# Performance work log

Hardware: AMD Instinct MI355X
Metric: run time of the kernel (lower is better)

## Reference

```python
import jax, jax.numpy as jnp
import numpy as np

EMBED_DIM = 256
NUM_HEADS = 8
HEAD_DIM = EMBED_DIM // NUM_HEADS
NUM_GRAPHS = 64
MAX_LEN = 512
EPS = 1e-5
SCALE = float(1.0 / np.sqrt(HEAD_DIM))


def setup_inputs() -> dict:
    rng = np.random.default_rng(0)
    lengths = rng.integers(256, MAX_LEN + 1, size=NUM_GRAPHS)  # variable graph sizes
    batch = jnp.asarray(np.repeat(np.arange(NUM_GRAPHS), lengths), dtype=jnp.int32)
    N = int(lengths.sum())
    key = jax.random.key(0)
    ks = jax.random.split(key, 4)
    s = float(1.0 / np.sqrt(EMBED_DIM))
    return dict(
        x=jax.random.normal(ks[0], (N, EMBED_DIM), jnp.float32),
        batch=batch,
        in_proj_w=jax.random.uniform(ks[1], (3 * EMBED_DIM, EMBED_DIM), jnp.float32, -s, s),
        in_proj_b=jnp.zeros((3 * EMBED_DIM,), jnp.float32),
        out_proj_w=jax.random.uniform(ks[2], (EMBED_DIM, EMBED_DIM), jnp.float32, -s, s),
        out_proj_b=jnp.zeros((EMBED_DIM,), jnp.float32),
        ln_weight=jnp.ones((EMBED_DIM,), jnp.float32),
        ln_bias=jnp.zeros((EMBED_DIM,), jnp.float32),
    )


def reference(x, batch, in_proj_w, in_proj_b, out_proj_w, out_proj_b, ln_weight, ln_bias):
    N, D = x.shape
    # --- to_dense_batch: pad variable-size graphs into [B, S, D] ---
    counts = jax.ops.segment_sum(jnp.ones((N,), jnp.int32), batch, num_segments=NUM_GRAPHS)
    starts = jnp.cumsum(counts) - counts
    pos = jnp.arange(N, dtype=jnp.int32) - starts[batch]  # position of node inside its graph
    dense = jnp.zeros((NUM_GRAPHS, MAX_LEN, D), x.dtype).at[batch, pos].set(x)
    mask = jnp.zeros((NUM_GRAPHS, MAX_LEN), bool).at[batch, pos].set(True)

    # --- masked multi-head self-attention (torch nn.MultiheadAttention semantics) ---
    qkv = dense @ in_proj_w.T + in_proj_b                      # [B, S, 3D]
    q, k, v = jnp.split(qkv, 3, axis=-1)
    hd = lambda t: t.reshape(NUM_GRAPHS, MAX_LEN, NUM_HEADS, HEAD_DIM)
    q, k, v = hd(q), hd(k), hd(v)
    scores = jnp.einsum('bqhd,bkhd->bhqk', q, k) * SCALE       # [B, H, S, S]
    scores = jnp.where(mask[:, None, None, :], scores, -1e9)   # key_padding_mask
    attn = jax.nn.softmax(scores, axis=-1)
    ctx = jnp.einsum('bhqk,bkhd->bqhd', attn, v).reshape(NUM_GRAPHS, MAX_LEN, D)
    out_dense = ctx @ out_proj_w.T + out_proj_b

    # --- gather back to ragged layout + residual ---
    h = out_dense[batch, pos] + x                              # [N, D]

    # --- PyG LayerNorm(mode='graph'): normalize over all nodes & channels per graph ---
    norm = jnp.clip(counts.astype(x.dtype), 1.0)[:, None] * D
    mean = jax.ops.segment_sum(h, batch, num_segments=NUM_GRAPHS).sum(-1, keepdims=True) / norm
    hc = h - mean[batch]
    var = jax.ops.segment_sum(hc * hc, batch, num_segments=NUM_GRAPHS).sum(-1, keepdims=True) / norm
    out = hc / jnp.sqrt(var + EPS)[batch]
    out = out * ln_weight + ln_bias

    # --- activation: exact (erf) GELU, matching torch nn.GELU default ---
    return jax.nn.gelu(out, approximate=False)
```

## Files before the change

### kernel.cpp

```cpp
#include <hip/hip_runtime.h>
#include <hip/hip_bf16.h>
#include <math.h>

#define D_EMB 256
#define NHEAD 8
#define HD 32
#define NG 64
#define QSC 0.25503486f

typedef __attribute__((ext_vector_type(8))) short short8b;
typedef __attribute__((ext_vector_type(4))) float f32x4;

__device__ __forceinline__ unsigned int pk2(float a, float b) {
    union { __hip_bfloat162 t; unsigned int u; } r;
    r.t = __float22bfloat162_rn(make_float2(a, b));
    return r.u;
}

__device__ __forceinline__ short8b pack2v(f32x4 a, f32x4 b) {
    union { unsigned int u[4]; short8b s; } r;
    r.u[0] = pk2(a[0], a[1]);
    r.u[1] = pk2(a[2], a[3]);
    r.u[2] = pk2(b[0], b[1]);
    r.u[3] = pk2(b[2], b[3]);
    return r.s;
}

__device__ __forceinline__ float fexp2(float x) {
    float r;
    asm("v_exp_f32 %0, %1" : "=v"(r) : "v"(x));
    return r;
}

__device__ __forceinline__ void barrier_lgkm() {
    asm volatile("s_waitcnt lgkmcnt(0)" ::: "memory");
    __builtin_amdgcn_s_barrier();
}

__global__ void k_init(const float* __restrict__ x, unsigned short* __restrict__ xb, int n4x,
                       const float* __restrict__ w1, unsigned short* __restrict__ wb1,
                       const float* __restrict__ w2, unsigned short* __restrict__ wb2,
                       const int* __restrict__ batch, int n, int* __restrict__ starts,
                       float* __restrict__ part) {
    int seg = blockIdx.y;
    int i = blockIdx.x * 256 + threadIdx.x;
    if (seg == 3) {
        if (i < n) {
            int b = batch[i];
            if (i == 0 || batch[i - 1] != b) starts[b] = i;
            if (i == n - 1) starts[NG] = n;
        }
        if (blockIdx.x == 0 && threadIdx.x < 128) part[threadIdx.x] = 0.f;
        return;
    }
    const float* src = seg == 0 ? x : (seg == 1 ? w1 : w2);
    unsigned short* dst = seg == 0 ? xb : (seg == 1 ? wb1 : wb2);
    int n4 = seg == 0 ? n4x : (seg == 1 ? 768 * 64 : 256 * 64);
    if (i >= n4) return;
    float4 v = ((const float4*)src)[i];
    uint2 o;
    o.x = pk2(v.x, v.y);
    o.y = pk2(v.z, v.w);
    ((uint2*)dst)[i] = o;
}

#define GLSW 72

template<int MODE>
__global__ __launch_bounds__(256) void k_gemm(
    const unsigned short* __restrict__ A, const unsigned short* __restrict__ W,
    const float* __restrict__ bias, const float* __restrict__ resid,
    float* __restrict__ Cf, unsigned short* __restrict__ Qb,
    unsigned short* __restrict__ Kb, unsigned short* __restrict__ Vb,
    const int* __restrict__ batch, float* __restrict__ part,
    int M, int Ncols) {
    __shared__ __align__(16) unsigned short Al[128][GLSW];
    __shared__ __align__(16) unsigned short Bl[128][GLSW];

    int tid = threadIdx.x;
    int wave = tid >> 6, lane = tid & 63;
    int lrow = lane & 15, lgrp = lane >> 4;
    int wr = wave >> 1, wc = wave & 1;
    int row0 = blockIdx.x * 128, col0 = blockIdx.y * 128;

    int sr = tid >> 3, sc = (tid & 7) * 8;
    int arow[4], brow[4];
#pragma unroll
    for (int p = 0; p < 4; ++p) {
        int r = sr + p * 32;
        int ar = row0 + r; if (ar >= M) ar = M - 1;
        arow[p] = ar;
        brow[p] = col0 + r;
    }

    f32x4 acc[4][4];
#pragma unroll
    for (int i = 0; i < 4; ++i)
#pragma unroll
        for (int j = 0; j < 4; ++j) acc[i][j] = (f32x4){0.f, 0.f, 0.f, 0.f};

    short8b pa[4], pb[4];
#pragma unroll
    for (int p = 0; p < 4; ++p) {
        pa[p] = *(const short8b*)&A[(size_t)arow[p] * 256 + sc];
        pb[p] = *(const short8b*)&W[(size_t)brow[p] * 256 + sc];
    }

    for (int k0 = 0; k0 < 256; k0 += 64) {
#pragma unroll
        for (int p = 0; p < 4; ++p) {
            int r = sr + p * 32;
            *(short8b*)&Al[r][sc] = pa[p];
            *(short8b*)&Bl[r][sc] = pb[p];
        }
        if (k0 + 64 < 256) {
#pragma unroll
            for (int p = 0; p < 4; ++p) {
                pa[p] = *(const short8b*)&A[(size_t)arow[p] * 256 + k0 + 64 + sc];
                pb[p] = *(const short8b*)&W[(size_t)brow[p] * 256 + k0 + 64 + sc];
            }
        }
        barrier_lgkm();
#pragma unroll
        for (int half = 0; half < 2; ++half) {
            short8b af[4], bf[4];
#pragma unroll
            for (int mi = 0; mi < 4; ++mi)
                af[mi] = *(const short8b*)&Al[wr * 64 + mi * 16 + lrow][half * 32 + lgrp * 8];
#pragma unroll
            for (int ni = 0; ni < 4; ++ni)
                bf[ni] = *(const short8b*)&Bl[wc * 64 + ni * 16 + lrow][half * 32 + lgrp * 8];
#pragma unroll
            for (int mi = 0; mi < 4; ++mi)
#pragma unroll
                for (int ni = 0; ni < 4; ++ni)
                    acc[mi][ni] = __builtin_amdgcn_mfma_f32_16x16x32_bf16(
                        af[mi], bf[ni], acc[mi][ni], 0, 0, 0);
        }
        barrier_lgkm();
    }

    if (MODE == 0) {
        int g0 = batch[row0 < M ? row0 : M - 1];
        int rlast = row0 + 127; if (rlast >= M) rlast = M - 1;
        int g1 = batch[rlast];
        float bv[4];
#pragma unroll
        for (int ni = 0; ni < 4; ++ni)
            bv[ni] = bias[col0 + wc * 64 + ni * 16 + lrow];
        float sA = 0.f, qA = 0.f, sB = 0.f, qB = 0.f;
#pragma unroll
        for (int mi = 0; mi < 4; ++mi) {
            int rowb = row0 + wr * 64 + mi * 16 + lgrp * 4;
#pragma unroll
            for (int r = 0; r < 4; ++r) {
                int row = rowb + r;
                if (row >= M) continue;
                float rs = 0.f, rq = 0.f;
#pragma unroll
                for (int ni = 0; ni < 4; ++ni) {
                    int col = col0 + wc * 64 + ni * 16 + lrow;
                    float v = acc[mi][ni][r] + bv[ni];
                    v += resid[(size_t)row * Ncols + col];
                    Cf[(size_t)row * Ncols + col] = v;
                    rs += v;
                    rq += v * v;
                }
                if (batch[row] == g0) { sA += rs; qA += rq; }
                else                  { sB += rs; qB += rq; }
            }
        }
#pragma unroll
        for (int o = 32; o > 0; o >>= 1) {
            sA += __shfl_down(sA, o); qA += __shfl_down(qA, o);
            sB += __shfl_down(sB, o); qB += __shfl_down(qB, o);
        }
        __shared__ float red[4][4];
        if (lane == 0) {
            red[wave][0] = sA; red[wave][1] = qA;
            red[wave][2] = sB; red[wave][3] = qB;
        }
        __syncthreads();
        if (tid == 0) {
            float tA = 0.f, uA = 0.f, tB = 0.f, uB = 0.f;
#pragma unroll
            for (int w = 0; w < 4; ++w) {
                tA += red[w][0]; uA += red[w][1];
                tB += red[w][2]; uB += red[w][3];
            }
            atomicAdd(&part[2 * g0], tA);
            atomicAdd(&part[2 * g0 + 1], uA);
            if (g1 != g0) {
                atomicAdd(&part[2 * g1], tB);
                atomicAdd(&part[2 * g1 + 1], uB);
            }
        }
    } else {
        int sel = blockIdx.y >> 1;
        unsigned short* dst = sel == 0 ? Qb : (sel == 1 ? Kb : Vb);
        float qsc = sel == 0 ? QSC : 1.f;
#pragma unroll
        for (int ni = 0; ni < 4; ++ni) {
            int colg = col0 + wc * 64 + ni * 16 + lrow;
            int col = colg & 255;
            float bvv = bias[colg];
#pragma unroll
            for (int mi = 0; mi < 4; ++mi) {
                int rowb = row0 + wr * 64 + mi * 16 + lgrp * 4;
#pragma unroll
                for (int r = 0; r < 4; ++r) {
                    int row = rowb + r;
                    if (row < M) {
                        union { __hip_bfloat16 b; unsigned short u; } cv;
                        cv.b = __float2bfloat16((acc[mi][ni][r] + bvv) * qsc);
                        dst[(size_t)row * 256 + col] = cv.u;
                    }
                }
            }
        }
    }
}

#define KSW 40
#define VSW 76

__global__ __launch_bounds__(256) void k_attn6(
    const unsigned short* __restrict__ Qb, const unsigned short* __restrict__ Kb,
    const unsigned short* __restrict__ Vb, const int* __restrict__ starts,
    unsigned short* __restrict__ ctxb) {
    int g = blockIdx.x, h = blockIdx.y, chunk = blockIdx.z;
    int s0 = starts[g];
    int L = starts[g + 1] - s0;
    if (chunk * 128 >= L) return;

    __shared__ __align__(16) unsigned short Klds[2][64][KSW];
    __shared__ __align__(16) unsigned short Vt[2][32][VSW];

    int tid = threadIdx.x;
    int wave = tid >> 6, lane = tid & 63;
    int lrow = lane & 15, lgrp = lane >> 4;
    int qbase = chunk * 128 + wave * 32;

    short8b qf[2];
#pragma unroll
    for (int qm = 0; qm < 2; ++qm) {
        int qr = qbase + qm * 16 + lrow;
        if (qr >= L) qr = L - 1;
        qf[qm] = *(const short8b*)&Qb[(size_t)(s0 + qr) * 256 + h * 32 + lgrp * 8];
    }

    int skey = tid >> 2, skc = (tid & 3) * 8;
    int vu = tid >> 3, vd4 = (tid & 7) * 4;

    short8b kreg;
    ushort4 vreg0, vreg1;
    {
        int kr = skey < L ? skey : L - 1;
        kreg = *(const short8b*)&Kb[(size_t)(s0 + kr) * 256 + h * 32 + skc];
        int v0 = (2 * vu) < L ? (2 * vu) : L - 1;
        int v1 = (2 * vu + 1) < L ? (2 * vu + 1) : L - 1;
        vreg0 = *(const ushort4*)&Vb[(size_t)(s0 + v0) * 256 + h * 32 + vd4];
        vreg1 = *(const ushort4*)&Vb[(size_t)(s0 + v1) * 256 + h * 32 + vd4];
    }

    float lrun[2] = {0.f, 0.f};
    f32x4 acc[2][2];
#pragma unroll
    for (int a = 0; a < 2; ++a) {
        acc[a][0] = (f32x4){0.f, 0.f, 0.f, 0.f};
        acc[a][1] = (f32x4){0.f, 0.f, 0.f, 0.f};
    }

    int nkt = (L + 63) >> 6;
    for (int t = 0; t < nkt; ++t) {
        int kt = t * 64;
        int buf = t & 1;

        *(short8b*)&Klds[buf][skey][skc] = kreg;
#pragma unroll
        for (int j = 0; j < 4; ++j) {
            unsigned int pr = (unsigned int)(unsigned short)(&vreg0.x)[j] |
                              ((unsigned int)(unsigned short)(&vreg1.x)[j] << 16);
            *(unsigned int*)&Vt[buf][vd4 + j][2 * vu] = pr;
        }

        if (t + 1 < nkt) {
            int ktn = kt + 64;
            int kr = (ktn + skey) < L ? (ktn + skey) : L - 1;
            kreg = *(const short8b*)&Kb[(size_t)(s0 + kr) * 256 + h * 32 + skc];
            int v0 = (ktn + 2 * vu) < L ? (ktn + 2 * vu) : L - 1;
            int v1 = (ktn + 2 * vu + 1) < L ? (ktn + 2 * vu + 1) : L - 1;
            vreg0 = *(const ushort4*)&Vb[(size_t)(s0 + v0) * 256 + h * 32 + vd4];
            vreg1 = *(const ushort4*)&Vb[(size_t)(s0 + v1) * 256 + h * 32 + vd4];
        }

        barrier_lgkm();

        short8b kf[4];
#pragma unroll
        for (int kn = 0; kn < 4; ++kn)
            kf[kn] = *(const short8b*)&Klds[buf][kn * 16 + lrow][lgrp * 8];
        short8b vf[2][2];
#pragma unroll
        for (int dsub = 0; dsub < 2; ++dsub)
#pragma unroll
            for (int kh = 0; kh < 2; ++kh) {
                ushort4 lo = *(const ushort4*)&Vt[buf][dsub * 16 + lrow][kh * 32 + lgrp * 4];
                ushort4 hi = *(const ushort4*)&Vt[buf][dsub * 16 + lrow][kh * 32 + 16 + lgrp * 4];
                union { ushort4 q[2]; short8b s; } u;
                u.q[0] = lo; u.q[1] = hi;
                vf[dsub][kh] = u.s;
            }

        bool tail = (kt + 64 > L);
        short8b pf[2][2];
#pragma unroll
        for (int qm = 0; qm < 2; ++qm) {
            f32x4 s[4];
#pragma unroll
            for (int kn = 0; kn < 4; ++kn)
                s[kn] = __builtin_amdgcn_mfma_f32_16x16x32_bf16(
                    kf[kn], qf[qm], (f32x4){0.f, 0.f, 0.f, 0.f}, 0, 0, 0);
            if (tail) {
#pragma unroll
                for (int kn = 0; kn < 4; ++kn)
#pragma unroll
                    for (int r = 0; r < 4; ++r) {
                        int key = kt + kn * 16 + lgrp * 4 + r;
                        if (key >= L) s[kn][r] = -INFINITY;
                    }
            }
            float psk[4];
#pragma unroll
            for (int kn = 0; kn < 4; ++kn) {
                float p0 = fexp2(fminf(s[kn][0], 80.f));
                float p1 = fexp2(fminf(s[kn][1], 80.f));
                float p2 = fexp2(fminf(s[kn][2], 80.f));
                float p3 = fexp2(fminf(s[kn][3], 80.f));
                s[kn][0] = p0; s[kn][1] = p1; s[kn][2] = p2; s[kn][3] = p3;
                psk[kn] = (p0 + p1) + (p2 + p3);
            }
            lrun[qm] += (psk[0] + psk[1]) + (psk[2] + psk[3]);
            pf[qm][0] = pack2v(s[0], s[1]);
            pf[qm][1] = pack2v(s[2], s[3]);
        }

#pragma unroll
        for (int qm = 0; qm < 2; ++qm)
#pragma unroll
            for (int dsub = 0; dsub < 2; ++dsub) {
                acc[qm][dsub] = __builtin_amdgcn_mfma_f32_16x16x32_bf16(
                    vf[dsub][0], pf[qm][0], acc[qm][dsub], 0, 0, 0);
                acc[qm][dsub] = __builtin_amdgcn_mfma_f32_16x16x32_bf16(
                    vf[dsub][1], pf[qm][1], acc[qm][dsub], 0, 0, 0);
            }
    }

#pragma unroll
    for (int qm = 0; qm < 2; ++qm) {
        int q = qbase + qm * 16 + lrow;
        float tsum = lrun[qm];
        tsum += __shfl_xor(tsum, 16);
        tsum += __shfl_xor(tsum, 32);
        if (q >= L) continue;
        float inv = 1.f / tsum;
        unsigned short* dst = ctxb + (size_t)(s0 + q) * 256 + h * 32;
#pragma unroll
        for (int dsub = 0; dsub < 2; ++dsub) {
#pragma unroll
            for (int rp = 0; rp < 4; rp += 2) {
                *(unsigned int*)&dst[dsub * 16 + lgrp * 4 + rp] =
                    pk2(acc[qm][dsub][rp] * inv, acc[qm][dsub][rp + 1] * inv);
            }
        }
    }
}

__global__ void k_stats_final(const float* __restrict__ part,
                              const int* __restrict__ starts,
                              float* __restrict__ stats) {
    int g = threadIdx.x;
    if (g >= NG) return;
    float S = part[2 * g], Q = part[2 * g + 1];
    float norm = (float)(starts[g + 1] - starts[g]) * (float)D_EMB;
    float mean = S / norm;
    float var = Q / norm - mean * mean;
    stats[2 * g] = mean;
    stats[2 * g + 1] = rsqrtf(var + 1e-5f);
}

__global__ void k_ln_gelu(float* __restrict__ h, const int* __restrict__ batch,
                          const float* __restrict__ stats, const float* __restrict__ lw,
                          const float* __restrict__ lb, int n) {
    int idx = blockIdx.x * blockDim.x + threadIdx.x;
    if (idx >= n * (D_EMB / 4)) return;
    int row = idx >> 6;
    int c4 = idx & 63;
    int g = batch[row];
    float mean = stats[2 * g], inv = stats[2 * g + 1];
    float4 v = *(float4*)&h[(size_t)idx * 4];
    float4 wv = *(const float4*)&lw[c4 * 4];
    float4 bv = *(const float4*)&lb[c4 * 4];
    float y;
    y = (v.x - mean) * inv * wv.x + bv.x; v.x = 0.5f * y * (1.f + erff(y * 0.70710678118f));
    y = (v.y - mean) * inv * wv.y + bv.y; v.y = 0.5f * y * (1.f + erff(y * 0.70710678118f));
    y = (v.z - mean) * inv * wv.z + bv.z; v.z = 0.5f * y * (1.f + erff(y * 0.70710678118f));
    y = (v.w - mean) * inv * wv.w + bv.w; v.w = 0.5f * y * (1.f + erff(y * 0.70710678118f));
    *(float4*)&h[(size_t)idx * 4] = v;
}

extern "C" void kernel_launch(void* const* d_in, const int* in_sizes, int n_in,
                              void* d_out, int out_size, void* d_ws, size_t ws_size,
                              hipStream_t stream) {
    const float* x     = (const float*)d_in[0];
    const int*   batch = (const int*)d_in[1];
    const float* in_w  = (const float*)d_in[2];
    const float* in_b  = (const float*)d_in[3];
    const float* out_w = (const float*)d_in[4];
    const float* out_b = (const float*)d_in[5];
    const float* ln_w  = (const float*)d_in[6];
    const float* ln_b  = (const float*)d_in[7];
    int N = in_sizes[1];
    float* out = (float*)d_out;

    char* ws = (char*)d_ws;
    int*   starts = (int*)ws;
    float* stats  = (float*)(ws + 512);
    float* part   = (float*)(ws + 1024);
    unsigned short* xb   = (unsigned short*)(ws + 3072);
    unsigned short* wb1  = xb + (size_t)N * 256;
    unsigned short* wb2  = wb1 + 768 * 256;
    unsigned short* Qb   = wb2 + 256 * 256;
    unsigned short* Kb   = Qb + (size_t)N * 256;
    unsigned short* Vb   = Kb + (size_t)N * 256;
    unsigned short* ctxb = Vb + (size_t)N * 256;

    int n4x = N * 64;
    k_init<<<dim3((n4x + 255) / 256, 4), 256, 0, stream>>>(
        x, xb, n4x, in_w, wb1, out_w, wb2, batch, N, starts, part);

    dim3 g1((N + 127) / 128, 6);
    k_gemm<1><<<g1, 256, 0, stream>>>(xb, wb1, in_b, nullptr, nullptr,
                                      Qb, Kb, Vb, nullptr, nullptr, N, 768);

    k_attn6<<<dim3(NG, NHEAD, 4), 256, 0, stream>>>(Qb, Kb, Vb, starts, ctxb);

    dim3 g3((N + 127) / 128, 2);
    k_gemm<0><<<g3, 256, 0, stream>>>(ctxb, wb2, out_b, x, out,
                                      nullptr, nullptr, nullptr, batch, part, N, 256);

    k_stats_final<<<1, 64, 0, stream>>>(part, starts, stats);

    int nv4 = N * (D_EMB / 4);
    k_ln_gelu<<<(nv4 + 255) / 256, 256, 0, stream>>>(out, batch, stats, ln_w, ln_b, N);
}
```

Before: 136.6 us.

## Fuse bf16 conversion into GEMMs, triple-buffer attention, fold stats into LN

After: 139.4 us. 1.02x slower.

```diff
diff --git a/kernel.cpp b/kernel.cpp
--- a/kernel.cpp
+++ b/kernel.cpp
@@ -26,54 +26,42 @@
     return r.s;
 }
 
+__device__ __forceinline__ short8b pack8fl(float4 a, float4 b) {
+    union { unsigned int u[4]; short8b s; } r;
+    r.u[0] = pk2(a.x, a.y);
+    r.u[1] = pk2(a.z, a.w);
+    r.u[2] = pk2(b.x, b.y);
+    r.u[3] = pk2(b.z, b.w);
+    return r.s;
+}
+
 __device__ __forceinline__ float fexp2(float x) {
     float r;
     asm("v_exp_f32 %0, %1" : "=v"(r) : "v"(x));
     return r;
 }
+__device__ __forceinline__ float frcp(float x) {
+    float r;
+    asm("v_rcp_f32 %0, %1" : "=v"(r) : "v"(x));
+    return r;
+}
 
 __device__ __forceinline__ void barrier_lgkm() {
     asm volatile("s_waitcnt lgkmcnt(0)" ::: "memory");
     __builtin_amdgcn_s_barrier();
 }
 
-__global__ void k_init(const float* __restrict__ x, unsigned short* __restrict__ xb, int n4x,
-                       const float* __restrict__ w1, unsigned short* __restrict__ wb1,
-                       const float* __restrict__ w2, unsigned short* __restrict__ wb2,
-                       const int* __restrict__ batch, int n, int* __restrict__ starts,
-                       float* __restrict__ part) {
-    int seg = blockIdx.y;
-    int i = blockIdx.x * 256 + threadIdx.x;
-    if (seg == 3) {
-        if (i < n) {
-            int b = batch[i];
-            if (i == 0 || batch[i - 1] != b) starts[b] = i;
-            if (i == n - 1) starts[NG] = n;
-        }
-        if (blockIdx.x == 0 && threadIdx.x < 128) part[threadIdx.x] = 0.f;
-        return;
-    }
-    const float* src = seg == 0 ? x : (seg == 1 ? w1 : w2);
-    unsigned short* dst = seg == 0 ? xb : (seg == 1 ? wb1 : wb2);
-    int n4 = seg == 0 ? n4x : (seg == 1 ? 768 * 64 : 256 * 64);
-    if (i >= n4) return;
-    float4 v = ((const float4*)src)[i];
-    uint2 o;
-    o.x = pk2(v.x, v.y);
-    o.y = pk2(v.z, v.w);
-    ((uint2*)dst)[i] = o;
-}
-
 #define GLSW 72
 
 template<int MODE>
 __global__ __launch_bounds__(256) void k_gemm(
-    const unsigned short* __restrict__ A, const unsigned short* __restrict__ W,
+    const unsigned short* __restrict__ Abf, const float* __restrict__ Af,
+    const float* __restrict__ Wf,
     const float* __restrict__ bias, const float* __restrict__ resid,
     float* __restrict__ Cf, unsigned short* __restrict__ Qb,
     unsigned short* __restrict__ Kb, unsigned short* __restrict__ Vb,
     const int* __restrict__ batch, float* __restrict__ part,
-    int M, int Ncols) {
+    int* __restrict__ starts, int M, int Ncols) {
     __shared__ __align__(16) unsigned short Al[128][GLSW];
     __shared__ __align__(16) unsigned short Bl[128][GLSW];
 
@@ -83,6 +71,16 @@
     int wr = wave >> 1, wc = wave & 1;
     int row0 = blockIdx.x * 128, col0 = blockIdx.y * 128;
 
+    if (MODE == 1 && blockIdx.y == 0) {
+        int i = row0 + tid;
+        if (tid < 128 && i < M) {
+            int b = batch[i];
+            if (i == 0 || batch[i - 1] != b) starts[b] = i;
+            if (i == M - 1) starts[NG] = M;
+        }
+        if (blockIdx.x == 0 && tid < 128) part[tid] = 0.f;
+    }
+
     int sr = tid >> 3, sc = (tid & 7) * 8;
     int arow[4], brow[4];
 #pragma unroll
@@ -99,25 +97,39 @@
 #pragma unroll
         for (int j = 0; j < 4; ++j) acc[i][j] = (f32x4){0.f, 0.f, 0.f, 0.f};
 
-    short8b pa[4], pb[4];
+    short8b pabf[4];
+    float4 pa0[4], pa1[4], pw0[4], pw1[4];
 #pragma unroll
     for (int p = 0; p < 4; ++p) {
-        pa[p] = *(const short8b*)&A[(size_t)arow[p] * 256 + sc];
-        pb[p] = *(const short8b*)&W[(size_t)brow[p] * 256 + sc];
+        if (MODE == 0) {
+            pabf[p] = *(const short8b*)&Abf[(size_t)arow[p] * 256 + sc];
+        } else {
+            const float4* ap = (const float4*)&Af[(size_t)arow[p] * 256 + sc];
+            pa0[p] = ap[0]; pa1[p] = ap[1];
+        }
+        const float4* wp = (const float4*)&Wf[(size_t)brow[p] * 256 + sc];
+        pw0[p] = wp[0]; pw1[p] = wp[1];
     }
 
     for (int k0 = 0; k0 < 256; k0 += 64) {
 #pragma unroll
         for (int p = 0; p < 4; ++p) {
             int r = sr + p * 32;
-            *(short8b*)&Al[r][sc] = pa[p];
-            *(short8b*)&Bl[r][sc] = pb[p];
+            if (MODE == 0) *(short8b*)&Al[r][sc] = pabf[p];
+            else           *(short8b*)&Al[r][sc] = pack8fl(pa0[p], pa1[p]);
+            *(short8b*)&Bl[r][sc] = pack8fl(pw0[p], pw1[p]);
         }
         if (k0 + 64 < 256) {
 #pragma unroll
             for (int p = 0; p < 4; ++p) {
-                pa[p] = *(const short8b*)&A[(size_t)arow[p] * 256 + k0 + 64 + sc];
-                pb[p] = *(const short8b*)&W[(size_t)brow[p] * 256 + k0 + 64 + sc];
+                if (MODE == 0) {
+                    pabf[p] = *(const short8b*)&Abf[(size_t)arow[p] * 256 + k0 + 64 + sc];
+                } else {
+                    const float4* ap = (const float4*)&Af[(size_t)arow[p] * 256 + k0 + 64 + sc];
+                    pa0[p] = ap[0]; pa1[p] = ap[1];
+                }
+                const float4* wp = (const float4*)&Wf[(size_t)brow[p] * 256 + k0 + 64 + sc];
+                pw0[p] = wp[0]; pw1[p] = wp[1];
             }
         }
         barrier_lgkm();
@@ -233,8 +245,8 @@
     int L = starts[g + 1] - s0;
     if (chunk * 128 >= L) return;
 
-    __shared__ __align__(16) unsigned short Klds[2][64][KSW];
-    __shared__ __align__(16) unsigned short Vt[2][32][VSW];
+    __shared__ __align__(16) unsigned short Klds[3][64][KSW];
+    __shared__ __align__(16) unsigned short Vt[3][32][VSW];
 
     int tid = threadIdx.x;
     int wave = tid >> 6, lane = tid & 63;
@@ -252,17 +264,6 @@
     int skey = tid >> 2, skc = (tid & 3) * 8;
     int vu = tid >> 3, vd4 = (tid & 7) * 4;
 
-    short8b kreg;
-    ushort4 vreg0, vreg1;
-    {
-        int kr = skey < L ? skey : L - 1;
-        kreg = *(const short8b*)&Kb[(size_t)(s0 + kr) * 256 + h * 32 + skc];
-        int v0 = (2 * vu) < L ? (2 * vu) : L - 1;
-        int v1 = (2 * vu + 1) < L ? (2 * vu + 1) : L - 1;
-        vreg0 = *(const ushort4*)&Vb[(size_t)(s0 + v0) * 256 + h * 32 + vd4];
-        vreg1 = *(const ushort4*)&Vb[(size_t)(s0 + v1) * 256 + h * 32 + vd4];
-    }
-
     float lrun[2] = {0.f, 0.f};
     f32x4 acc[2][2];
 #pragma unroll
@@ -272,46 +273,40 @@
     }
 
     int nkt = (L + 63) >> 6;
-    for (int t = 0; t < nkt; ++t) {
-        int kt = t * 64;
-        int buf = t & 1;
-
-        *(short8b*)&Klds[buf][skey][skc] = kreg;
+
+    auto LOADSET = [&](short8b& kr, ushort4& v0, ushort4& v1, int kt) {
+        int r0 = (kt + skey) < L ? (kt + skey) : L - 1;
+        kr = *(const short8b*)&Kb[(size_t)(s0 + r0) * 256 + h * 32 + skc];
+        int r1 = (kt + 2 * vu) < L ? (kt + 2 * vu) : L - 1;
+        int r2 = (kt + 2 * vu + 1) < L ? (kt + 2 * vu + 1) : L - 1;
+        v0 = *(const ushort4*)&Vb[(size_t)(s0 + r1) * 256 + h * 32 + vd4];
+        v1 = *(const ushort4*)&Vb[(size_t)(s0 + r2) * 256 + h * 32 + vd4];
+    };
+    auto WRITESET = [&](short8b& kr, ushort4& v0, ushort4& v1, int bi) {
+        *(short8b*)&Klds[bi][skey][skc] = kr;
 #pragma unroll
         for (int j = 0; j < 4; ++j) {
-            unsigned int pr = (unsigned int)(unsigned short)(&vreg0.x)[j] |
-                              ((unsigned int)(unsigned short)(&vreg1.x)[j] << 16);
-            *(unsigned int*)&Vt[buf][vd4 + j][2 * vu] = pr;
-        }
-
-        if (t + 1 < nkt) {
-            int ktn = kt + 64;
-            int kr = (ktn + skey) < L ? (ktn + skey) : L - 1;
-            kreg = *(const short8b*)&Kb[(size_t)(s0 + kr) * 256 + h * 32 + skc];
-            int v0 = (ktn + 2 * vu) < L ? (ktn + 2 * vu) : L - 1;
-            int v1 = (ktn + 2 * vu + 1) < L ? (ktn + 2 * vu + 1) : L - 1;
-            vreg0 = *(const ushort4*)&Vb[(size_t)(s0 + v0) * 256 + h * 32 + vd4];
-            vreg1 = *(const ushort4*)&Vb[(size_t)(s0 + v1) * 256 + h * 32 + vd4];
-        }
-
-        barrier_lgkm();
-
+            unsigned int pr = (unsigned int)(unsigned short)(&v0.x)[j] |
+                              ((unsigned int)(unsigned short)(&v1.x)[j] << 16);
+            *(unsigned int*)&Vt[bi][vd4 + j][2 * vu] = pr;
+        }
+    };
+    auto COMPUTE = [&](int kt, int bi) {
         short8b kf[4];
 #pragma unroll
         for (int kn = 0; kn < 4; ++kn)
-            kf[kn] = *(const short8b*)&Klds[buf][kn * 16 + lrow][lgrp * 8];
+            kf[kn] = *(const short8b*)&Klds[bi][kn * 16 + lrow][lgrp * 8];
         short8b vf[2][2];
 #pragma unroll
         for (int dsub = 0; dsub < 2; ++dsub)
 #pragma unroll
             for (int kh = 0; kh < 2; ++kh) {
-                ushort4 lo = *(const ushort4*)&Vt[buf][dsub * 16 + lrow][kh * 32 + lgrp * 4];
-                ushort4 hi = *(const ushort4*)&Vt[buf][dsub * 16 + lrow][kh * 32 + 16 + lgrp * 4];
+                ushort4 lo = *(const ushort4*)&Vt[bi][dsub * 16 + lrow][kh * 32 + lgrp * 4];
+                ushort4 hi = *(const ushort4*)&Vt[bi][dsub * 16 + lrow][kh * 32 + 16 + lgrp * 4];
                 union { ushort4 q[2]; short8b s; } u;
                 u.q[0] = lo; u.q[1] = hi;
                 vf[dsub][kh] = u.s;
             }
-
         bool tail = (kt + 64 > L);
         short8b pf[2][2];
 #pragma unroll
@@ -344,7 +339,6 @@
             pf[qm][0] = pack2v(s[0], s[1]);
             pf[qm][1] = pack2v(s[2], s[3]);
         }
-
 #pragma unroll
         for (int qm = 0; qm < 2; ++qm)
 #pragma unroll
@@ -354,6 +348,30 @@
                 acc[qm][dsub] = __builtin_amdgcn_mfma_f32_16x16x32_bf16(
                     vf[dsub][1], pf[qm][1], acc[qm][dsub], 0, 0, 0);
             }
+    };
+
+    short8b k0r, k1r, k2r;
+    ushort4 a0, b0, a1, b1, a2, b2;
+    LOADSET(k0r, a0, b0, 0);
+    LOADSET(k1r, a1, b1, 64);
+    LOADSET(k2r, a2, b2, 128);
+    WRITESET(k0r, a0, b0, 0);
+
+    for (int t = 0; t < nkt; t += 3) {
+        if (t + 1 < nkt) WRITESET(k1r, a1, b1, 1);
+        if (t + 3 < nkt) LOADSET(k0r, a0, b0, (t + 3) * 64);
+        barrier_lgkm();
+        COMPUTE(t * 64, 0);
+        if (t + 1 >= nkt) break;
+        if (t + 2 < nkt) WRITESET(k2r, a2, b2, 2);
+        if (t + 4 < nkt) LOADSET(k1r, a1, b1, (t + 4) * 64);
+        barrier_lgkm();
+        COMPUTE((t + 1) * 64, 1);
+        if (t + 2 >= nkt) break;
+        if (t + 3 < nkt) WRITESET(k0r, a0, b0, 0);
+        if (t + 5 < nkt) LOADSET(k2r, a2, b2, (t + 5) * 64);
+        barrier_lgkm();
+        COMPUTE((t + 2) * 64, 2);
     }
 
 #pragma unroll
@@ -376,36 +394,35 @@
     }
 }
 
-__global__ void k_stats_final(const float* __restrict__ part,
-                              const int* __restrict__ starts,
-                              float* __restrict__ stats) {
-    int g = threadIdx.x;
-    if (g >= NG) return;
-    float S = part[2 * g], Q = part[2 * g + 1];
-    float norm = (float)(starts[g + 1] - starts[g]) * (float)D_EMB;
-    float mean = S / norm;
-    float var = Q / norm - mean * mean;
-    stats[2 * g] = mean;
-    stats[2 * g + 1] = rsqrtf(var + 1e-5f);
+__device__ __forceinline__ float gelu_erf(float y) {
+    float ax = fabsf(y) * 0.70710678118f;
+    float t = frcp(1.f + 0.3275911f * ax);
+    float poly = t * (0.254829592f + t * (-0.284496736f +
+                 t * (1.421413741f + t * (-1.453152027f + t * 1.061405429f))));
+    float e = fexp2(-ax * ax * 1.44269504f);
+    float erf = 1.f - poly * e;
+    erf = __builtin_copysignf(erf, y);
+    return 0.5f * y * (1.f + erf);
 }
 
 __global__ void k_ln_gelu(float* __restrict__ h, const int* __restrict__ batch,
-                          const float* __restrict__ stats, const float* __restrict__ lw,
-                          const float* __restrict__ lb, int n) {
+                          const float* __restrict__ part, const int* __restrict__ starts,
+                          const float* __restrict__ lw, const float* __restrict__ lb, int n) {
     int idx = blockIdx.x * blockDim.x + threadIdx.x;
     if (idx >= n * (D_EMB / 4)) return;
     int row = idx >> 6;
     int c4 = idx & 63;
     int g = batch[row];
-    float mean = stats[2 * g], inv = stats[2 * g + 1];
+    float rn = frcp((float)(starts[g + 1] - starts[g]) * (float)D_EMB);
+    float mean = part[2 * g] * rn;
+    float inv = rsqrtf(part[2 * g + 1] * rn - mean * mean + 1e-5f);
     float4 v = *(float4*)&h[(size_t)idx * 4];
     float4 wv = *(const float4*)&lw[c4 * 4];
     float4 bv = *(const float4*)&lb[c4 * 4];
-    float y;
-    y = (v.x - mean) * inv * wv.x + bv.x; v.x = 0.5f * y * (1.f + erff(y * 0.70710678118f));
-    y = (v.y - mean) * inv * wv.y + bv.y; v.y = 0.5f * y * (1.f + erff(y * 0.70710678118f));
-    y = (v.z - mean) * inv * wv.z + bv.z; v.z = 0.5f * y * (1.f + erff(y * 0.70710678118f));
-    y = (v.w - mean) * inv * wv.w + bv.w; v.w = 0.5f * y * (1.f + erff(y * 0.70710678118f));
+    v.x = gelu_erf((v.x - mean) * inv * wv.x + bv.x);
+    v.y = gelu_erf((v.y - mean) * inv * wv.y + bv.y);
+    v.z = gelu_erf((v.z - mean) * inv * wv.z + bv.z);
+    v.w = gelu_erf((v.w - mean) * inv * wv.w + bv.w);
     *(float4*)&h[(size_t)idx * 4] = v;
 }
 
@@ -425,32 +442,24 @@
 
     char* ws = (char*)d_ws;
     int*   starts = (int*)ws;
-    float* stats  = (float*)(ws + 512);
-    float* part   = (float*)(ws + 1024);
-    unsigned short* xb   = (unsigned short*)(ws + 3072);
-    unsigned short* wb1  = xb + (size_t)N * 256;
-    unsigned short* wb2  = wb1 + 768 * 256;
-    unsigned short* Qb   = wb2 + 256 * 256;
+    float* part   = (float*)(ws + 512);
+    unsigned short* Qb   = (unsigned short*)(ws + 2048);
     unsigned short* Kb   = Qb + (size_t)N * 256;
     unsigned short* Vb   = Kb + (size_t)N * 256;
     unsigned short* ctxb = Vb + (size_t)N * 256;
 
-    int n4x = N * 64;
-    k_init<<<dim3((n4x + 255) / 256, 4), 256, 0, stream>>>(
-        x, xb, n4x, in_w, wb1, out_w, wb2, batch, N, starts, part);
-
     dim3 g1((N + 127) / 128, 6);
-    k_gemm<1><<<g1, 256, 0, stream>>>(xb, wb1, in_b, nullptr, nullptr,
-                                      Qb, Kb, Vb, nullptr, nullptr, N, 768);
+    k_gemm<1><<<g1, 256, 0, stream>>>(nullptr, x, in_w, in_b, nullptr, nullptr,
+                                      Qb, Kb, Vb, batch, part, starts, N, 768);
 
     k_attn6<<<dim3(NG, NHEAD, 4), 256, 0, stream>>>(Qb, Kb, Vb, starts, ctxb);
 
     dim3 g3((N + 127) / 128, 2);
-    k_gemm<0><<<g3, 256, 0, stream>>>(ctxb, wb2, out_b, x, out,
-                                      nullptr, nullptr, nullptr, batch, part, N, 256);
-
-    k_stats_final<<<1, 64, 0, stream>>>(part, starts, stats);
+    k_gemm<0><<<g3, 256, 0, stream>>>(ctxb, nullptr, out_w, out_b, x, out,
+                                      nullptr, nullptr, nullptr, batch, part,
+                                      starts, N, 256);
 
     int nv4 = N * (D_EMB / 4);
-    k_ln_gelu<<<(nv4 + 255) / 256, 256, 0, stream>>>(out, batch, stats, ln_w, ln_b, N);
-}
+    k_ln_gelu<<<(nv4 + 255) / 256, 256, 0, stream>>>(out, batch, part, starts,
+                                                     ln_w, ln_b, N);
+}
```
